# Kernel optimization log

Measured on AMD Instinct MI355X. Metric: run time of the kernel, lower is better.

The kernel has to match this reference:

```python
import jax, jax.numpy as jnp
import numpy as np

N = 40000; E = 512000; F = 128; H = 4; C = 32; HC = 128; G = 64; FC = 48


def _bn(x, g, b):
    # BatchNorm1d in training mode: batch stats, biased variance, eps=1e-5
    mu = jnp.mean(x, 0)
    var = jnp.var(x, 0)
    return g * (x - mu) * jax.lax.rsqrt(var + 1e-5) + b


def _gat(x, src, dst, W, a_s, a_d, bias):
    # PyG GATConv: linear -> per-head edge scores -> self-loops -> LeakyReLU ->
    # segment softmax over incoming edges of each target -> weighted scatter-add
    n = x.shape[0]
    h = (x @ W).reshape(n, H, C)
    es = jnp.einsum('nhc,hc->nh', h, a_s)  # source-side score
    ed = jnp.einsum('nhc,hc->nh', h, a_d)  # target-side score
    loop = jnp.arange(n, dtype=src.dtype)
    s = jnp.concatenate([src, loop])
    d = jnp.concatenate([dst, loop])
    e = jax.nn.leaky_relu(es[s] + ed[d], 0.2)  # [E+N, H]
    m = jax.ops.segment_max(e, d, num_segments=n)
    ex = jnp.exp(e - m[d])
    den = jax.ops.segment_sum(ex, d, num_segments=n)
    alpha = ex / den[d]
    out = jax.ops.segment_sum(h[s] * alpha[:, :, None], d, num_segments=n)
    return out.reshape(n, H * C) + bias


def _pool(x, batch, aw, ab):
    # graph_attention_pool: per-graph softmax over node scores, weighted scatter-add
    sc = x @ aw + ab  # [N,1]
    m = jax.ops.segment_max(sc, batch, num_segments=G)
    ex = jnp.exp(sc - m[batch])
    den = jax.ops.segment_sum(ex, batch, num_segments=G)
    a = ex / den[batch]
    return jax.ops.segment_sum(x * a, batch, num_segments=G)  # [G, HC]


def _forward(x1, x2, W0, as0, ad0, b0, W1, as1, ad1, b1, W2, as2, ad2, b2,
             g1, be1, g2, be2, g3, be3, att_w, att_b, fci_w, fci_b, gbi, bbi,
             fcw, fcb, fc1w, fc1b, gf1, bf1, fc2w, fc2b,
             edge_index1, batch1, edge_index2, batch2):
    def branch(x, ei):
        src, dst = ei[0], ei[1]
        x = jax.nn.relu(_bn(_gat(x, src, dst, W0, as0, ad0, b0), g1, be1))
        x = jax.nn.relu(_bn(_gat(x, src, dst, W1, as1, ad1, b1), g2, be2))
        x = jax.nn.relu(_bn(_gat(x, src, dst, W2, as2, ad2, b2), g3, be3))
        return x
    h1 = branch(x1, edge_index1)
    h2 = branch(x2, edge_index2)
    def head(h, batch):
        p = _pool(h, batch, att_w, att_b)
        z = jax.nn.relu(_bn(p @ fci_w + fci_b, gbi, bbi))
        return z @ fcw + fcb  # note: bn_fc is never applied in the source forward
    o = jnp.concatenate([head(h1, batch1), head(h2, batch2)], axis=-1)
    o = jax.nn.relu(_bn(o @ fc1w + fc1b, gf1, bf1))
    o = o @ fc2w + fc2b
    return jax.nn.sigmoid(o).squeeze(-1)  # [G]


def setup_inputs() -> dict:
    key = jax.random.key(0)
    ks = jax.random.split(key, 24)
    def rn(i, shape, scale=1.0):
        return jax.random.normal(ks[i], shape, jnp.float32) * scale
    inp = {}
    inp['x1'] = rn(0, (N, F))
    inp['x2'] = rn(1, (N, F))
    inp['edge_index1'] = jax.random.randint(ks[2], (2, E), 0, N, dtype=jnp.int32)
    inp['edge_index2'] = jax.random.randint(ks[3], (2, E), 0, N, dtype=jnp.int32)
    inp['batch1'] = jnp.sort(jax.random.randint(ks[4], (N,), 0, G, dtype=jnp.int32))
    inp['batch2'] = jnp.sort(jax.random.randint(ks[5], (N,), 0, G, dtype=jnp.int32))
    inp['W0'] = rn(6, (F, HC), F ** -0.5)
    inp['as0'] = rn(7, (H, C), C ** -0.5)
    inp['ad0'] = rn(8, (H, C), C ** -0.5)
    inp['b0'] = jnp.zeros((HC,), jnp.float32)
    inp['W1'] = rn(9, (HC, HC), HC ** -0.5)
    inp['as1'] = rn(10, (H, C), C ** -0.5)
    inp['ad1'] = rn(11, (H, C), C ** -0.5)
    inp['b1'] = jnp.zeros((HC,), jnp.float32)
    inp['W2'] = rn(12, (HC, HC), HC ** -0.5)
    inp['as2'] = rn(13, (H, C), C ** -0.5)
    inp['ad2'] = rn(14, (H, C), C ** -0.5)
    inp['b2'] = jnp.zeros((HC,), jnp.float32)
    for nm, dim in (('g1', HC), ('g2', HC), ('g3', HC), ('gbi', FC), ('gf1', FC // 4)):
        inp[nm] = jnp.ones((dim,), jnp.float32)
    for nm, dim in (('be1', HC), ('be2', HC), ('be3', HC), ('bbi', FC), ('bf1', FC // 4)):
        inp[nm] = jnp.zeros((dim,), jnp.float32)
    inp['att_w'] = rn(15, (HC, 1), HC ** -0.5)
    inp['att_b'] = jnp.zeros((1,), jnp.float32)
    inp['fci_w'] = rn(16, (HC, FC), HC ** -0.5)
    inp['fci_b'] = jnp.zeros((FC,), jnp.float32)
    inp['fcw'] = rn(17, (FC, FC // 4), FC ** -0.5)
    inp['fcb'] = jnp.zeros((FC // 4,), jnp.float32)
    inp['fc1w'] = rn(18, (FC // 4 * 2, FC // 4), (FC // 2) ** -0.5)
    inp['fc1b'] = jnp.zeros((FC // 4,), jnp.float32)
    inp['fc2w'] = rn(19, (FC // 4, 1), (FC // 4) ** -0.5)
    inp['fc2b'] = jnp.zeros((1,), jnp.float32)
    return inp


def reference(x1, x2, edge_index1, edge_index2, batch1, batch2,
              W0, as0, ad0, b0, W1, as1, ad1, b1, W2, as2, ad2, b2,
              g1, g2, g3, gbi, gf1, be1, be2, be3, bbi, bf1,
              att_w, att_b, fci_w, fci_b, fcw, fcb, fc1w, fc1b, fc2w, fc2b):
    return _forward(x1, x2, W0, as0, ad0, b0, W1, as1, ad1, b1, W2, as2, ad2, b2,
                    g1, be1, g2, be2, g3, be3, att_w, att_b, fci_w, fci_b, gbi, bbi,
                    fcw, fcb, fc1w, fc1b, gf1, bf1, fc2w, fc2b,
                    edge_index1, batch1, edge_index2, batch2)
```

## Files before the change

kernel.cpp:

```cpp
#include <hip/hip_runtime.h>

#define NN 40000
#define EE 512000
#define NB 157
#define BCAP 8000

typedef unsigned short u16;
typedef __attribute__((ext_vector_type(8))) short bf16x8;
typedef __attribute__((ext_vector_type(4))) float f32x4;

__device__ __forceinline__ float bf2f(u16 u) { return __uint_as_float(((unsigned)u) << 16); }
__device__ __forceinline__ u16 f2bf(float f) {
    unsigned u = __float_as_uint(f);
    u += 0x7FFFu + ((u >> 16) & 1u);
    return (u16)(u >> 16);
}
__device__ __forceinline__ unsigned pack2(float a, float b) {
    return (unsigned)f2bf(a) | ((unsigned)f2bf(b) << 16);
}
__device__ __forceinline__ float lrelu(float t) { return t > 0.f ? t : 0.2f * t; }

__global__ __launch_bounds__(256) void detect_k(const u16* __restrict__ x, int* __restrict__ flag) {
    int t = threadIdx.x;
    int cnt = 0;
    for (int j = 0; j < 8; ++j) {
        float v = bf2f(x[(t * 8 + j) * 2]);
        float a = fabsf(v);
        if (a >= 0.00390625f && a <= 256.0f) cnt++;
    }
    __shared__ int sh[256];
    sh[t] = cnt;
    __syncthreads();
    for (int off = 128; off > 0; off >>= 1) {
        if (t < off) sh[t] += sh[t + off];
        __syncthreads();
    }
    if (t == 0) flag[0] = (sh[0] > 1024) ? 1 : 0;
}

struct CvtArgs {
    const void* src[28];
    float* dst[28];
    int n[28];
};

__global__ __launch_bounds__(256) void cvt_k(CvtArgs a, const int* __restrict__ flag) {
    int b = blockIdx.x;
    int n = a.n[b];
    float* d = a.dst[b];
    if (*flag) {
        const u16* p = (const u16*)a.src[b];
        for (int i = threadIdx.x; i < n; i += 256) d[i] = bf2f(p[i]);
    } else {
        const float* p = (const float*)a.src[b];
        for (int i = threadIdx.x; i < n; i += 256) d[i] = p[i];
    }
}

__global__ __launch_bounds__(256) void wtb_k(const float* __restrict__ wcvt, u16* __restrict__ Wtb) {
    int l = blockIdx.x;
    const float* W = wcvt + l * 16640;
    u16* D = Wtb + l * 16384;
    for (int i = threadIdx.x; i < 16384; i += 256) {
        int n = i >> 7, k = i & 127;
        D[i] = f2bf(W[k * 128 + n]);
    }
}

__global__ __launch_bounds__(256) void bucket_k(const int* __restrict__ ei,
                                                int* __restrict__ gcnt,
                                                int2* __restrict__ buf) {
    __shared__ int lh[NB];
    __shared__ int lbase[NB];
    __shared__ int loff[NB];
    int tid = threadIdx.x;
    for (int i = tid; i < NB; i += 256) lh[i] = 0;
    __syncthreads();
    int e0 = blockIdx.x * 1024 + tid;
    int sv[4], dv[4], bv[4];
#pragma unroll
    for (int j = 0; j < 4; ++j) {
        int e = e0 + j * 256;
        int d = ei[EE + e];
        int s = ei[e];
        if ((unsigned)d >= NN) d = -1;
        if ((unsigned)s >= NN) s = 0;
        dv[j] = d;
        sv[j] = s;
        bv[j] = d >> 8;
        if (d >= 0 && (unsigned)bv[j] < NB) atomicAdd(&lh[bv[j]], 1);
        else dv[j] = -1;
    }
    __syncthreads();
    for (int i = tid; i < NB; i += 256) {
        int c = lh[i];
        lbase[i] = c ? atomicAdd(&gcnt[i], c) : 0;
        loff[i] = 0;
    }
    __syncthreads();
#pragma unroll
    for (int j = 0; j < 4; ++j) {
        if (dv[j] >= 0) {
            int b = bv[j];
            int p = lbase[b] + atomicAdd(&loff[b], 1);
            if ((unsigned)p < BCAP) buf[b * BCAP + p] = (int2){sv[j], dv[j]};
        }
    }
}

__global__ __launch_bounds__(256) void build_k(const int* __restrict__ gcnt,
                                               const int2* __restrict__ buf,
                                               int* __restrict__ fill,
                                               int* __restrict__ csrc) {
    __shared__ int lf[256];
    int b = blockIdx.x, tid = threadIdx.x;
    lf[tid] = 0;
    __syncthreads();
    int n = gcnt[b];
    if (n < 0) n = 0;
    if (n > BCAP) n = BCAP;
    int d0 = b << 8;
    for (int i = tid; i < n; i += 256) {
        int2 p = buf[b * BCAP + i];
        unsigned loc = (unsigned)(p.y - d0);
        if (loc < 256u && (unsigned)p.y < NN && (unsigned)p.x < NN) {
            int pos = atomicAdd(&lf[loc], 1);
            if ((unsigned)pos < 64u) csrc[(size_t)p.y * 64 + pos] = p.x;
        }
    }
    __syncthreads();
    int d = d0 + tid;
    if (d < NN) fill[d] = lf[tid];
}

__global__ __launch_bounds__(256) void matmul_mfma_k(const void* __restrict__ Xv, int mode,
                                                     const int* __restrict__ flag,
                                                     const float* __restrict__ bkt,
                                                     const float* __restrict__ gam,
                                                     const float* __restrict__ bet,
                                                     const u16* __restrict__ Wtb,
                                                     const float* __restrict__ asf,
                                                     const float* __restrict__ adf,
                                                     u16* __restrict__ Yb,
                                                     float* __restrict__ es, float* __restrict__ ed) {
    __shared__ u16 Xs[64 * 136];
    __shared__ float red[256];
    __shared__ float scs[128], shs[128];
    int tid = threadIdx.x;
    size_t row0 = (size_t)blockIdx.x * 64;
    if (mode == 1) {
        float s = 0.f;
        for (int b = 0; b < 64; ++b) s += bkt[b * 256 + tid];
        red[tid] = s;
        __syncthreads();
        if (tid < 128) {
            float mu = red[tid] * (1.0f / NN);
            float var = red[128 + tid] * (1.0f / NN) - mu * mu;
            float sc_ = rsqrtf(var + 1e-5f) * gam[tid];
            scs[tid] = sc_;
            shs[tid] = bet[tid] - mu * sc_;
        }
        __syncthreads();
        const uint2* X2 = reinterpret_cast<const uint2*>((const u16*)Xv + row0 * 128);
        for (int i = tid; i < 2048; i += 256) {
            uint2 p = X2[i];
            int r = i >> 5, c0 = (i & 31) * 4;
            float v0 = fmaf(bf2f((u16)(p.x & 0xffffu)), scs[c0], shs[c0]);
            float v1 = fmaf(bf2f((u16)(p.x >> 16)), scs[c0 + 1], shs[c0 + 1]);
            float v2 = fmaf(bf2f((u16)(p.y & 0xffffu)), scs[c0 + 2], shs[c0 + 2]);
            float v3 = fmaf(bf2f((u16)(p.y >> 16)), scs[c0 + 3], shs[c0 + 3]);
            v0 = v0 > 0.f ? v0 : 0.f; v1 = v1 > 0.f ? v1 : 0.f;
            v2 = v2 > 0.f ? v2 : 0.f; v3 = v3 > 0.f ? v3 : 0.f;
            unsigned* dst = (unsigned*)(Xs + r * 136 + c0);
            dst[0] = pack2(v0, v1);
            dst[1] = pack2(v2, v3);
        }
    } else if (*flag) {
        const uint2* X2 = reinterpret_cast<const uint2*>((const u16*)Xv + row0 * 128);
        for (int i = tid; i < 2048; i += 256) {
            uint2 p = X2[i];
            int r = i >> 5, c0 = (i & 31) * 4;
            unsigned* dst = (unsigned*)(Xs + r * 136 + c0);
            dst[0] = p.x;
            dst[1] = p.y;
        }
    } else {
        const float4* X4 = reinterpret_cast<const float4*>((const float*)Xv + row0 * 128);
        for (int i = tid; i < 2048; i += 256) {
            float4 v = X4[i];
            int r = i >> 5, c0 = (i & 31) * 4;
            unsigned* dst = (unsigned*)(Xs + r * 136 + c0);
            dst[0] = pack2(v.x, v.y);
            dst[1] = pack2(v.z, v.w);
        }
    }
    __syncthreads();
    int w = tid >> 6, l = tid & 63;
    int q = l >> 4, c = l & 15;
    int mrow = w * 16;
    f32x4 acc[8];
#pragma unroll
    for (int t = 0; t < 8; ++t) acc[t] = (f32x4){0.f, 0.f, 0.f, 0.f};
#pragma unroll
    for (int ks = 0; ks < 4; ++ks) {
        int k0 = ks * 32;
        bf16x8 afrag = *(const bf16x8*)(Xs + (mrow + c) * 136 + k0 + q * 8);
#pragma unroll
        for (int t = 0; t < 8; ++t) {
            bf16x8 bfrag = *(const bf16x8*)(Wtb + (t * 16 + c) * 128 + k0 + q * 8);
            acc[t] = __builtin_amdgcn_mfma_f32_16x16x32_bf16(afrag, bfrag, acc[t], 0, 0, 0);
        }
    }
    float esp[4][4] = {}, edp[4][4] = {};
#pragma unroll
    for (int t = 0; t < 8; ++t) {
        float av = asf[t * 16 + c], dv = adf[t * 16 + c];
        int h = t >> 1;
#pragma unroll
        for (int r = 0; r < 4; ++r) {
            esp[h][r] = fmaf(acc[t][r], av, esp[h][r]);
            edp[h][r] = fmaf(acc[t][r], dv, edp[h][r]);
        }
    }
#pragma unroll
    for (int h = 0; h < 4; ++h)
#pragma unroll
        for (int r = 0; r < 4; ++r) {
            esp[h][r] += __shfl_xor(esp[h][r], 1, 64);
            esp[h][r] += __shfl_xor(esp[h][r], 2, 64);
            esp[h][r] += __shfl_xor(esp[h][r], 4, 64);
            esp[h][r] += __shfl_xor(esp[h][r], 8, 64);
            edp[h][r] += __shfl_xor(edp[h][r], 1, 64);
            edp[h][r] += __shfl_xor(edp[h][r], 2, 64);
            edp[h][r] += __shfl_xor(edp[h][r], 4, 64);
            edp[h][r] += __shfl_xor(edp[h][r], 8, 64);
        }
    if (c < 4) {
#pragma unroll
        for (int r = 0; r < 4; ++r) {
            size_t row = row0 + mrow + q * 4 + r;
            es[row * 4 + c] = esp[c][r];
            ed[row * 4 + c] = edp[c][r];
        }
    }
    __syncthreads();
    u16* Cs = Xs;
#pragma unroll
    for (int t = 0; t < 8; ++t)
#pragma unroll
        for (int r = 0; r < 4; ++r)
            Cs[(mrow + q * 4 + r) * 128 + t * 16 + c] = f2bf(acc[t][r]);
    __syncthreads();
    uint2* yp = (uint2*)(Yb + row0 * 128);
    const uint2* cs2 = (const uint2*)Cs;
    for (int i = tid; i < 2048; i += 256) yp[i] = cs2[i];
}

__global__ __launch_bounds__(256) void agg_k(const u16* __restrict__ hb, const float* __restrict__ es,
                                             const float* __restrict__ ed, const int* __restrict__ fill,
                                             const int* __restrict__ csrc, u16* __restrict__ Ab,
                                             float* __restrict__ bkt) {
    __shared__ float ss[512], qq[512];
    int wid = (blockIdx.x * 256 + threadIdx.x) >> 6;
    int lane = threadIdx.x & 63;
    int deg = fill[wid];
    if (deg > 64) deg = 64;
    if (deg < 0) deg = 0;
    int rs = wid * 64;
    int head = lane >> 4;
    float edn = ed[wid * 4 + head];
    float acc0, acc1, den;
    {
        float w = __expf(lrelu(es[wid * 4 + head] + edn));
        den = w;
        unsigned pv = ((const unsigned*)(hb + (size_t)wid * 128))[lane];
        acc0 = w * bf2f((u16)(pv & 0xffffu));
        acc1 = w * bf2f((u16)(pv >> 16));
    }
    int i = 0;
    for (; i + 8 <= deg; i += 8) {
        int sv[8];
#pragma unroll
        for (int j = 0; j < 8; ++j) sv[j] = csrc[rs + i + j];
        float wv[8];
#pragma unroll
        for (int j = 0; j < 8; ++j) wv[j] = __expf(lrelu(es[sv[j] * 4 + head] + edn));
        unsigned pv[8];
#pragma unroll
        for (int j = 0; j < 8; ++j) pv[j] = ((const unsigned*)(hb + (size_t)sv[j] * 128))[lane];
#pragma unroll
        for (int j = 0; j < 8; ++j) {
            den += wv[j];
            acc0 = fmaf(wv[j], bf2f((u16)(pv[j] & 0xffffu)), acc0);
            acc1 = fmaf(wv[j], bf2f((u16)(pv[j] >> 16)), acc1);
        }
    }
    for (; i < deg; ++i) {
        int s = csrc[rs + i];
        float w = __expf(lrelu(es[s * 4 + head] + edn));
        den += w;
        unsigned pv = ((const unsigned*)(hb + (size_t)s * 128))[lane];
        acc0 = fmaf(w, bf2f((u16)(pv & 0xffffu)), acc0);
        acc1 = fmaf(w, bf2f((u16)(pv >> 16)), acc1);
    }
    float inv = 1.0f / den;
    float v0 = acc0 * inv, v1 = acc1 * inv;
    ((unsigned*)Ab)[(size_t)wid * 64 + lane] = (unsigned)f2bf(v0) | ((unsigned)f2bf(v1) << 16);
    int w = threadIdx.x >> 6;
    ss[w * 128 + 2 * lane] = v0;      ss[w * 128 + 2 * lane + 1] = v1;
    qq[w * 128 + 2 * lane] = v0 * v0; qq[w * 128 + 2 * lane + 1] = v1 * v1;
    __syncthreads();
    int t = threadIdx.x;
    float* dst = bkt + (blockIdx.x & 63) * 256;
    if (t < 128) {
        atomicAdd(&dst[t], ss[t] + ss[128 + t] + ss[256 + t] + ss[384 + t]);
    } else {
        int f = t - 128;
        atomicAdd(&dst[t], qq[f] + qq[128 + f] + qq[256 + f] + qq[384 + f]);
    }
}

__global__ __launch_bounds__(256) void bnconst_k(const float* __restrict__ bkt,
                                                 const float* __restrict__ gam,
                                                 const float* __restrict__ bet,
                                                 float* __restrict__ bnc) {
    __shared__ float red[256];
    int tid = threadIdx.x;
    float s = 0.f;
    for (int b = 0; b < 64; ++b) s += bkt[b * 256 + tid];
    red[tid] = s;
    __syncthreads();
    if (tid < 128) {
        float mu = red[tid] * (1.0f / NN);
        float var = red[128 + tid] * (1.0f / NN) - mu * mu;
        float sc_ = rsqrtf(var + 1e-5f) * gam[tid];
        bnc[tid] = sc_;
        bnc[128 + tid] = bet[tid] - mu * sc_;
    }
}

__global__ __launch_bounds__(256) void pool_score_k(const u16* __restrict__ Ab,
                                                    const float* __restrict__ bnc,
                                                    const float* __restrict__ attw,
                                                    float* __restrict__ scw) {
    int tid = threadIdx.x;
    int wid = (blockIdx.x * 256 + tid) >> 6;
    int lane = tid & 63;
    int f0 = 2 * lane, f1 = 2 * lane + 1;
    unsigned pv = ((const unsigned*)Ab)[(size_t)wid * 64 + lane];
    float v0 = fmaf(bf2f((u16)(pv & 0xffffu)), bnc[f0], bnc[128 + f0]); v0 = v0 > 0.f ? v0 : 0.f;
    float v1 = fmaf(bf2f((u16)(pv >> 16)), bnc[f1], bnc[128 + f1]);     v1 = v1 > 0.f ? v1 : 0.f;
    float v = v0 * attw[f0] + v1 * attw[f1];
    for (int off = 1; off < 64; off <<= 1) v += __shfl_xor(v, off, 64);
    if (lane == 0) scw[wid] = __expf(v);
}

__device__ __forceinline__ int lower_bound_dev(const int* __restrict__ b, int n, int v) {
    int lo = 0, hi = n;
    while (lo < hi) {
        int mid = (lo + hi) >> 1;
        if (b[mid] < v) lo = mid + 1; else hi = mid;
    }
    return lo;
}

__global__ __launch_bounds__(256) void pool_den_k(const float* __restrict__ scw,
                                                  const int* __restrict__ batch,
                                                  float* __restrict__ gden) {
    int g = blockIdx.x;
    int tid = threadIdx.x;
    int start = lower_bound_dev(batch, NN, g);
    int end = lower_bound_dev(batch, NN, g + 1);
    __shared__ float sh[256];
    float s = 0.f;
    for (int i = start + tid; i < end; i += 256) s += scw[i];
    sh[tid] = s;
    __syncthreads();
    for (int off = 128; off > 0; off >>= 1) {
        if (tid < off) sh[tid] += sh[tid + off];
        __syncthreads();
    }
    if (tid == 0) gden[g] = (sh[0] > 1e-30f) ? sh[0] : 1e-30f;
}

__global__ __launch_bounds__(256) void pool_accum2_k(const u16* __restrict__ Ab,
                                                     const float* __restrict__ scw,
                                                     const int* __restrict__ batch,
                                                     const float* __restrict__ gden,
                                                     const float* __restrict__ bnc,
                                                     float* __restrict__ pooled) {
    __shared__ float wsh[64];
    __shared__ int gsh[64];
    int r0 = blockIdx.x * 64;
    int tid = threadIdx.x;
    if (tid < 64) {
        int g = batch[r0 + tid];
        if ((unsigned)g >= 64) g = 0;
        gsh[tid] = g;
        wsh[tid] = scw[r0 + tid] / gden[g];
    }
    __syncthreads();
    int f = tid & 127, half = tid >> 7;
    float bs = bnc[f], bb = bnc[128 + f];
    float racc = 0.f;
    int curg = gsh[half];
    for (int r = half; r < 64; r += 2) {
        int g = gsh[r];
        if (g != curg) {
            atomicAdd(&pooled[curg * 128 + f], racc);
            racc = 0.f;
            curg = g;
        }
        float v = fmaf(bf2f(Ab[(size_t)(r0 + r) * 128 + f]), bs, bb);
        v = v > 0.f ? v : 0.f;
        racc = fmaf(wsh[r], v, racc);
    }
    atomicAdd(&pooled[curg * 128 + f], racc);
}

__global__ __launch_bounds__(256) void headA_k(const float* __restrict__ pooled,
                                               const float* __restrict__ fciw, const float* __restrict__ fcib,
                                               float* __restrict__ Tall) {
    __shared__ float Wl[6144];
    __shared__ float Pl[128];
    int tid = threadIdx.x;
    int g = blockIdx.x;
    for (int i = tid; i < 6144; i += 256) Wl[i] = fciw[i];
    if (tid < 128) Pl[tid] = pooled[g * 128 + tid];
    __syncthreads();
    if (tid < 48) {
        float s = fcib[tid];
        for (int k = 0; k < 128; ++k) s = fmaf(Pl[k], Wl[k * 48 + tid], s);
        Tall[g * 48 + tid] = s;
    }
}

__global__ __launch_bounds__(256) void headB_k(const float* __restrict__ Tall,
                                               const float* __restrict__ gbi, const float* __restrict__ bbi,
                                               const float* __restrict__ fcw, const float* __restrict__ fcb,
                                               const float* __restrict__ fc1w, const float* __restrict__ fc1b,
                                               const float* __restrict__ gf1, const float* __restrict__ bf1,
                                               const float* __restrict__ fc2w, const float* __restrict__ fc2b,
                                               void* __restrict__ out, const int* __restrict__ flag) {
    __shared__ float T[6144];
    __shared__ float X[64 * 24];
    __shared__ float Y[64 * 12];
    __shared__ float st[192];
    __shared__ float st2[24];
    __shared__ float wl[576 + 288 + 12 + 12 + 12 + 12 + 48 + 48 + 1];
    float* fcw_l  = wl;
    float* fc1w_l = wl + 576;
    float* fcb_l  = wl + 864;
    float* fc1b_l = wl + 876;
    float* gf1_l  = wl + 888;
    float* bf1_l  = wl + 900;
    float* gbi_l  = wl + 912;
    float* bbi_l  = wl + 960;
    float* fc2b_l = wl + 1008;
    __shared__ float fc2w_l[12];
    int tid = threadIdx.x;
    for (int i = tid; i < 6144; i += 256) T[i] = Tall[i];
    for (int i = tid; i < 576; i += 256) fcw_l[i] = fcw[i];
    for (int i = tid; i < 288; i += 256) fc1w_l[i] = fc1w[i];
    if (tid < 12) {
        fcb_l[tid] = fcb[tid]; fc1b_l[tid] = fc1b[tid];
        gf1_l[tid] = gf1[tid]; bf1_l[tid] = bf1[tid];
        fc2w_l[tid] = fc2w[tid];
    }
    if (tid < 48) { gbi_l[tid] = gbi[tid]; bbi_l[tid] = bbi[tid]; }
    if (tid == 0) fc2b_l[0] = fc2b[0];
    __syncthreads();
    if (tid < 96) {
        int b = tid / 48, c = tid - b * 48;
        float s = 0.f, ss = 0.f;
        for (int g = 0; g < 64; ++g) { float v = T[b * 3072 + g * 48 + c]; s += v; ss += v * v; }
        float mu = s * (1.f / 64), var = ss * (1.f / 64) - mu * mu;
        float sc_ = rsqrtf(var + 1e-5f) * gbi_l[c];
        st[tid] = sc_;
        st[96 + tid] = bbi_l[c] - mu * sc_;
    }
    __syncthreads();
    for (int i = tid; i < 6144; i += 256) {
        int b = i / 3072, c = i % 48;
        int col = b * 48 + c;
        float v = fmaf(T[i], st[col], st[96 + col]);
        T[i] = v > 0.f ? v : 0.f;
    }
    __syncthreads();
    for (int idx = tid; idx < 1536; idx += 256) {
        int b = idx / 768, r = idx - b * 768;
        int g = r / 12, c = r - g * 12;
        float s = fcb_l[c];
        const float* tr = T + b * 3072 + g * 48;
        for (int k = 0; k < 48; ++k) s = fmaf(tr[k], fcw_l[k * 12 + c], s);
        X[g * 24 + b * 12 + c] = s;
    }
    __syncthreads();
    for (int idx = tid; idx < 768; idx += 256) {
        int g = idx / 12, c = idx - g * 12;
        float s = fc1b_l[c];
        const float* xr = X + g * 24;
        for (int k = 0; k < 24; ++k) s = fmaf(xr[k], fc1w_l[k * 12 + c], s);
        Y[idx] = s;
    }
    __syncthreads();
    if (tid < 12) {
        float s = 0.f, ss = 0.f;
        for (int g = 0; g < 64; ++g) { float v = Y[g * 12 + tid]; s += v; ss += v * v; }
        float mu = s * (1.f / 64), var = ss * (1.f / 64) - mu * mu;
        float sc_ = rsqrtf(var + 1e-5f) * gf1_l[tid];
        st2[tid] = sc_;
        st2[12 + tid] = bf1_l[tid] - mu * sc_;
    }
    __syncthreads();
    if (tid < 64) {
        float s = fc2b_l[0];
        for (int k = 0; k < 12; ++k) {
            float v = fmaf(Y[tid * 12 + k], st2[k], st2[12 + k]);
            v = v > 0.f ? v : 0.f;
            s = fmaf(v, fc2w_l[k], s);
        }
        float sig = 1.f / (1.f + __expf(-s));
        if (*flag) ((u16*)out)[tid] = f2bf(sig);
        else       ((float*)out)[tid] = sig;
    }
}

extern "C" void kernel_launch(void* const* d_in, const int* in_sizes, int n_in,
                              void* d_out, int out_size, void* d_ws, size_t ws_size,
                              hipStream_t stream) {
    const void* xin[2]  = {d_in[0], d_in[1]};
    const int* ei[2]    = {(const int*)d_in[2], (const int*)d_in[3]};
    const int* batch[2] = {(const int*)d_in[4], (const int*)d_in[5]};

    char* ws = (char*)d_ws;
    u16*   Hb     = (u16*)(ws + 0);
    u16*   Ab     = (u16*)(ws + 10240000);
    float* es     = (float*)(ws + 20480000);
    float* ed     = (float*)(ws + 21120000);
    float* scw    = (float*)(ws + 21760000);
    int*   fill   = (int*)(ws + 21920000);
    int*   csrc   = (int*)(ws + 22080000);
    float* wcvt   = (float*)(ws + 32320000);
    u16*   Wtb    = (u16*)(ws + 32560000);
    float* zbase  = (float*)(ws + 32658304);
    float* bkt    = zbase;
    float* pooled = zbase + 98304;
    float* gden   = pooled + 16384;
    float* bnc    = gden + 128;
    float* Tall   = bnc + 256;
    int*   flag   = (int*)(Tall + 6144);
    int*   gcnt   = (int*)scw;

    static const int widx[28] = {6,7,8, 10,11,12, 14,15,16, 18,19,20, 23,24,25,
                                 21,26, 22,27, 28, 30,31, 32,33, 34,35, 36,37};
    static const int wn[28]   = {16384,128,128, 16384,128,128, 16384,128,128, 128,128,128,
                                 128,128,128, 48,48, 12,12, 128, 6144,48, 576,12, 288,12, 12,1};
    CvtArgs ca;
    float* wptr[28];
    {
        size_t off = 0;
        for (int i = 0; i < 28; ++i) {
            ca.src[i] = d_in[widx[i]];
            ca.dst[i] = wcvt + off;
            ca.n[i] = wn[i];
            wptr[i] = wcvt + off;
            off += wn[i];
        }
    }
    const float* asf[3] = {wptr[1], wptr[4], wptr[7]};
    const float* adf[3] = {wptr[2], wptr[5], wptr[8]};
    const float* gf[3]  = {wptr[9], wptr[10], wptr[11]};
    const float* bef[3] = {wptr[12], wptr[13], wptr[14]};
    const float *gbi = wptr[15], *bbi = wptr[16], *gf1 = wptr[17], *bf1 = wptr[18];
    const float *attw = wptr[19], *fciw = wptr[20], *fcib = wptr[21];
    const float *fcw = wptr[22], *fcb = wptr[23], *fc1w = wptr[24], *fc1b = wptr[25];
    const float *fc2w = wptr[26], *fc2b = wptr[27];

    detect_k<<<1, 256, 0, stream>>>((const u16*)d_in[0], flag);
    cvt_k<<<28, 256, 0, stream>>>(ca, flag);
    wtb_k<<<3, 256, 0, stream>>>(wcvt, Wtb);
    (void)hipMemsetAsync(zbase, 0, (98304 + 16384) * sizeof(float), stream);

    for (int b = 0; b < 2; ++b) {
        (void)hipMemsetAsync(gcnt, 0, NB * sizeof(int), stream);
        bucket_k<<<500, 256, 0, stream>>>(ei[b], gcnt, (int2*)Hb);
        build_k<<<NB, 256, 0, stream>>>(gcnt, (const int2*)Hb, fill, csrc);
        for (int l = 0; l < 3; ++l) {
            float* bktl = bkt + (b * 3 + l) * 16384;
            float* bktprev = bkt + (b * 3 + l - 1) * 16384;
            matmul_mfma_k<<<625, 256, 0, stream>>>(l == 0 ? xin[b] : (const void*)Ab,
                                                   l == 0 ? 0 : 1, flag,
                                                   l == 0 ? bkt : bktprev,
                                                   l == 0 ? gf[0] : gf[l - 1],
                                                   l == 0 ? bef[0] : bef[l - 1],
                                                   Wtb + l * 16384, asf[l], adf[l], Hb, es, ed);
            agg_k<<<10000, 256, 0, stream>>>(Hb, es, ed, fill, csrc, Ab, bktl);
        }
        float* bkt3 = bkt + (b * 3 + 2) * 16384;
        bnconst_k<<<1, 256, 0, stream>>>(bkt3, gf[2], bef[2], bnc);
        pool_score_k<<<10000, 256, 0, stream>>>(Ab, bnc, attw, scw);
        pool_den_k<<<64, 256, 0, stream>>>(scw, batch[b], gden + b * 64);
        pool_accum2_k<<<625, 256, 0, stream>>>(Ab, scw, batch[b], gden + b * 64,
                                               bnc, pooled + b * 8192);
        headA_k<<<64, 256, 0, stream>>>(pooled + b * 8192, fciw, fcib, Tall + b * 3072);
    }
    headB_k<<<1, 256, 0, stream>>>(Tall, gbi, bbi, fcw, fcb, fc1w, fc1b, gf1, bf1,
                                   fc2w, fc2b, d_out, flag);
}
```

Before: 689.2 us.

## Batch both graph branches into single kernel launches per stage

Processes the two independent graph branches together: every stage (bucketing, CSR build, matmul, aggregation, pooling, head) launches once with twice the blocks, and each block picks its branch from its block index. Workspace buffers are doubled to hold both branches at once. BN constants are now computed by a separate small kernel after each layer instead of being recomputed inside every matmul block. This removes half the launches and gives small kernels more parallel work, at the cost of a larger workspace footprint.

```diff
diff --git a/kernel.cpp b/kernel.cpp
--- a/kernel.cpp
+++ b/kernel.cpp
@@ -67,16 +67,21 @@
     }
 }
 
-__global__ __launch_bounds__(256) void bucket_k(const int* __restrict__ ei,
+__global__ __launch_bounds__(256) void bucket_k(const int* __restrict__ ei1,
+                                                const int* __restrict__ ei2,
                                                 int* __restrict__ gcnt,
                                                 int2* __restrict__ buf) {
     __shared__ int lh[NB];
     __shared__ int lbase[NB];
     __shared__ int loff[NB];
+    int branch = blockIdx.x >= 500;
+    int blk = blockIdx.x - (branch ? 500 : 0);
+    const int* ei = branch ? ei2 : ei1;
+    int gb0 = branch * NB;
     int tid = threadIdx.x;
     for (int i = tid; i < NB; i += 256) lh[i] = 0;
     __syncthreads();
-    int e0 = blockIdx.x * 1024 + tid;
+    int e0 = blk * 1024 + tid;
     int sv[4], dv[4], bv[4];
 #pragma unroll
     for (int j = 0; j < 4; ++j) {
@@ -94,7 +99,7 @@
     __syncthreads();
     for (int i = tid; i < NB; i += 256) {
         int c = lh[i];
-        lbase[i] = c ? atomicAdd(&gcnt[i], c) : 0;
+        lbase[i] = c ? atomicAdd(&gcnt[gb0 + i], c) : 0;
         loff[i] = 0;
     }
     __syncthreads();
@@ -103,7 +108,7 @@
         if (dv[j] >= 0) {
             int b = bv[j];
             int p = lbase[b] + atomicAdd(&loff[b], 1);
-            if ((unsigned)p < BCAP) buf[b * BCAP + p] = (int2){sv[j], dv[j]};
+            if ((unsigned)p < BCAP) buf[(size_t)(gb0 + b) * BCAP + p] = (int2){sv[j], dv[j]};
         }
     }
 }
@@ -113,57 +118,57 @@
                                                int* __restrict__ fill,
                                                int* __restrict__ csrc) {
     __shared__ int lf[256];
-    int b = blockIdx.x, tid = threadIdx.x;
+    int branch = blockIdx.x >= NB;
+    int b = blockIdx.x - (branch ? NB : 0);
+    int tid = threadIdx.x;
     lf[tid] = 0;
     __syncthreads();
-    int n = gcnt[b];
+    int n = gcnt[branch * NB + b];
     if (n < 0) n = 0;
     if (n > BCAP) n = BCAP;
     int d0 = b << 8;
+    size_t soff = (size_t)branch * NN;
+    const int2* bp = buf + (size_t)(branch * NB + b) * BCAP;
     for (int i = tid; i < n; i += 256) {
-        int2 p = buf[b * BCAP + i];
+        int2 p = bp[i];
         unsigned loc = (unsigned)(p.y - d0);
         if (loc < 256u && (unsigned)p.y < NN && (unsigned)p.x < NN) {
             int pos = atomicAdd(&lf[loc], 1);
-            if ((unsigned)pos < 64u) csrc[(size_t)p.y * 64 + pos] = p.x;
+            if ((unsigned)pos < 64u) csrc[(soff + p.y) * 64 + pos] = p.x;
         }
     }
     __syncthreads();
     int d = d0 + tid;
-    if (d < NN) fill[d] = lf[tid];
-}
-
-__global__ __launch_bounds__(256) void matmul_mfma_k(const void* __restrict__ Xv, int mode,
+    if (d < NN) fill[soff + d] = lf[tid];
+}
+
+__global__ __launch_bounds__(256) void matmul_mfma_k(const void* __restrict__ X1,
+                                                     const void* __restrict__ X2,
+                                                     const u16* __restrict__ Abase,
+                                                     int mode,
                                                      const int* __restrict__ flag,
-                                                     const float* __restrict__ bkt,
-                                                     const float* __restrict__ gam,
-                                                     const float* __restrict__ bet,
+                                                     const float* __restrict__ bnc,
                                                      const u16* __restrict__ Wtb,
                                                      const float* __restrict__ asf,
                                                      const float* __restrict__ adf,
-                                                     u16* __restrict__ Yb,
+                                                     u16* __restrict__ Hbase,
                                                      float* __restrict__ es, float* __restrict__ ed) {
     __shared__ u16 Xs[64 * 136];
-    __shared__ float red[256];
     __shared__ float scs[128], shs[128];
     int tid = threadIdx.x;
-    size_t row0 = (size_t)blockIdx.x * 64;
+    int branch = blockIdx.x >= 625;
+    int blk = blockIdx.x - (branch ? 625 : 0);
+    size_t boff = (size_t)branch * NN;
+    size_t row0 = (size_t)blk * 64;
     if (mode == 1) {
-        float s = 0.f;
-        for (int b = 0; b < 64; ++b) s += bkt[b * 256 + tid];
-        red[tid] = s;
+        if (tid < 128) {
+            scs[tid] = bnc[branch * 256 + tid];
+            shs[tid] = bnc[branch * 256 + 128 + tid];
+        }
         __syncthreads();
-        if (tid < 128) {
-            float mu = red[tid] * (1.0f / NN);
-            float var = red[128 + tid] * (1.0f / NN) - mu * mu;
-            float sc_ = rsqrtf(var + 1e-5f) * gam[tid];
-            scs[tid] = sc_;
-            shs[tid] = bet[tid] - mu * sc_;
-        }
-        __syncthreads();
-        const uint2* X2 = reinterpret_cast<const uint2*>((const u16*)Xv + row0 * 128);
+        const uint2* X2p = reinterpret_cast<const uint2*>(Abase + (boff + row0) * 128);
         for (int i = tid; i < 2048; i += 256) {
-            uint2 p = X2[i];
+            uint2 p = X2p[i];
             int r = i >> 5, c0 = (i & 31) * 4;
             float v0 = fmaf(bf2f((u16)(p.x & 0xffffu)), scs[c0], shs[c0]);
             float v1 = fmaf(bf2f((u16)(p.x >> 16)), scs[c0 + 1], shs[c0 + 1]);
@@ -175,23 +180,26 @@
             dst[0] = pack2(v0, v1);
             dst[1] = pack2(v2, v3);
         }
-    } else if (*flag) {
-        const uint2* X2 = reinterpret_cast<const uint2*>((const u16*)Xv + row0 * 128);
-        for (int i = tid; i < 2048; i += 256) {
-            uint2 p = X2[i];
-            int r = i >> 5, c0 = (i & 31) * 4;
-            unsigned* dst = (unsigned*)(Xs + r * 136 + c0);
-            dst[0] = p.x;
-            dst[1] = p.y;
-        }
     } else {
-        const float4* X4 = reinterpret_cast<const float4*>((const float*)Xv + row0 * 128);
-        for (int i = tid; i < 2048; i += 256) {
-            float4 v = X4[i];
-            int r = i >> 5, c0 = (i & 31) * 4;
-            unsigned* dst = (unsigned*)(Xs + r * 136 + c0);
-            dst[0] = pack2(v.x, v.y);
-            dst[1] = pack2(v.z, v.w);
+        const void* Xv = branch ? X2 : X1;
+        if (*flag) {
+            const uint2* X2p = reinterpret_cast<const uint2*>((const u16*)Xv + row0 * 128);
+            for (int i = tid; i < 2048; i += 256) {
+                uint2 p = X2p[i];
+                int r = i >> 5, c0 = (i & 31) * 4;
+                unsigned* dst = (unsigned*)(Xs + r * 136 + c0);
+                dst[0] = p.x;
+                dst[1] = p.y;
+            }
+        } else {
+            const float4* X4 = reinterpret_cast<const float4*>((const float*)Xv + row0 * 128);
+            for (int i = tid; i < 2048; i += 256) {
+                float4 v = X4[i];
+                int r = i >> 5, c0 = (i & 31) * 4;
+                unsigned* dst = (unsigned*)(Xs + r * 136 + c0);
+                dst[0] = pack2(v.x, v.y);
+                dst[1] = pack2(v.z, v.w);
+            }
         }
     }
     __syncthreads();
@@ -238,9 +246,9 @@
     if (c < 4) {
 #pragma unroll
         for (int r = 0; r < 4; ++r) {
-            size_t row = row0 + mrow + q * 4 + r;
-            es[row * 4 + c] = esp[c][r];
-            ed[row * 4 + c] = edp[c][r];
+            size_t grow = boff + row0 + mrow + q * 4 + r;
+            es[grow * 4 + c] = esp[c][r];
+            ed[grow * 4 + c] = edp[c][r];
         }
     }
     __syncthreads();
@@ -251,7 +259,7 @@
         for (int r = 0; r < 4; ++r)
             Cs[(mrow + q * 4 + r) * 128 + t * 16 + c] = f2bf(acc[t][r]);
     __syncthreads();
-    uint2* yp = (uint2*)(Yb + row0 * 128);
+    uint2* yp = (uint2*)(Hbase + (boff + row0) * 128);
     const uint2* cs2 = (const uint2*)Cs;
     for (int i = tid; i < 2048; i += 256) yp[i] = cs2[i];
 }
@@ -259,21 +267,23 @@
 __global__ __launch_bounds__(256) void agg_k(const u16* __restrict__ hb, const float* __restrict__ es,
                                              const float* __restrict__ ed, const int* __restrict__ fill,
                                              const int* __restrict__ csrc, u16* __restrict__ Ab,
-                                             float* __restrict__ bkt) {
+                                             float* __restrict__ bktbase, int l) {
     __shared__ float ss[512], qq[512];
-    int wid = (blockIdx.x * 256 + threadIdx.x) >> 6;
+    int gwid = (blockIdx.x * 256 + threadIdx.x) >> 6;
+    int branch = gwid >= NN;
+    size_t srow = branch ? (size_t)NN : 0;
     int lane = threadIdx.x & 63;
-    int deg = fill[wid];
+    int deg = fill[gwid];
     if (deg > 64) deg = 64;
     if (deg < 0) deg = 0;
-    int rs = wid * 64;
+    size_t rs = (size_t)gwid * 64;
     int head = lane >> 4;
-    float edn = ed[wid * 4 + head];
+    float edn = ed[gwid * 4 + head];
     float acc0, acc1, den;
     {
-        float w = __expf(lrelu(es[wid * 4 + head] + edn));
+        float w = __expf(lrelu(es[gwid * 4 + head] + edn));
         den = w;
-        unsigned pv = ((const unsigned*)(hb + (size_t)wid * 128))[lane];
+        unsigned pv = ((const unsigned*)(hb + (size_t)gwid * 128))[lane];
         acc0 = w * bf2f((u16)(pv & 0xffffu));
         acc1 = w * bf2f((u16)(pv >> 16));
     }
@@ -284,10 +294,10 @@
         for (int j = 0; j < 8; ++j) sv[j] = csrc[rs + i + j];
         float wv[8];
 #pragma unroll
-        for (int j = 0; j < 8; ++j) wv[j] = __expf(lrelu(es[sv[j] * 4 + head] + edn));
+        for (int j = 0; j < 8; ++j) wv[j] = __expf(lrelu(es[(srow + sv[j]) * 4 + head] + edn));
         unsigned pv[8];
 #pragma unroll
-        for (int j = 0; j < 8; ++j) pv[j] = ((const unsigned*)(hb + (size_t)sv[j] * 128))[lane];
+        for (int j = 0; j < 8; ++j) pv[j] = ((const unsigned*)(hb + (srow + sv[j]) * 128))[lane];
 #pragma unroll
         for (int j = 0; j < 8; ++j) {
             den += wv[j];
@@ -297,21 +307,21 @@
     }
     for (; i < deg; ++i) {
         int s = csrc[rs + i];
-        float w = __expf(lrelu(es[s * 4 + head] + edn));
+        float w = __expf(lrelu(es[(srow + s) * 4 + head] + edn));
         den += w;
-        unsigned pv = ((const unsigned*)(hb + (size_t)s * 128))[lane];
+        unsigned pv = ((const unsigned*)(hb + (srow + s) * 128))[lane];
         acc0 = fmaf(w, bf2f((u16)(pv & 0xffffu)), acc0);
         acc1 = fmaf(w, bf2f((u16)(pv >> 16)), acc1);
     }
     float inv = 1.0f / den;
     float v0 = acc0 * inv, v1 = acc1 * inv;
-    ((unsigned*)Ab)[(size_t)wid * 64 + lane] = (unsigned)f2bf(v0) | ((unsigned)f2bf(v1) << 16);
+    ((unsigned*)Ab)[(size_t)gwid * 64 + lane] = (unsigned)f2bf(v0) | ((unsigned)f2bf(v1) << 16);
     int w = threadIdx.x >> 6;
     ss[w * 128 + 2 * lane] = v0;      ss[w * 128 + 2 * lane + 1] = v1;
     qq[w * 128 + 2 * lane] = v0 * v0; qq[w * 128 + 2 * lane + 1] = v1 * v1;
     __syncthreads();
     int t = threadIdx.x;
-    float* dst = bkt + (blockIdx.x & 63) * 256;
+    float* dst = bktbase + (branch * 3 + l) * 16384 + (blockIdx.x & 63) * 256;
     if (t < 128) {
         atomicAdd(&dst[t], ss[t] + ss[128 + t] + ss[256 + t] + ss[384 + t]);
     } else {
@@ -320,22 +330,24 @@
     }
 }
 
-__global__ __launch_bounds__(256) void bnconst_k(const float* __restrict__ bkt,
+__global__ __launch_bounds__(256) void bnconst_k(const float* __restrict__ bktbase, int l,
                                                  const float* __restrict__ gam,
                                                  const float* __restrict__ bet,
                                                  float* __restrict__ bnc) {
     __shared__ float red[256];
+    int b = blockIdx.x;
+    const float* bkt = bktbase + (b * 3 + l) * 16384;
     int tid = threadIdx.x;
     float s = 0.f;
-    for (int b = 0; b < 64; ++b) s += bkt[b * 256 + tid];
+    for (int k = 0; k < 64; ++k) s += bkt[k * 256 + tid];
     red[tid] = s;
     __syncthreads();
     if (tid < 128) {
         float mu = red[tid] * (1.0f / NN);
         float var = red[128 + tid] * (1.0f / NN) - mu * mu;
         float sc_ = rsqrtf(var + 1e-5f) * gam[tid];
-        bnc[tid] = sc_;
-        bnc[128 + tid] = bet[tid] - mu * sc_;
+        bnc[b * 256 + tid] = sc_;
+        bnc[b * 256 + 128 + tid] = bet[tid] - mu * sc_;
     }
 }
 
@@ -344,15 +356,17 @@
                                                     const float* __restrict__ attw,
                                                     float* __restrict__ scw) {
     int tid = threadIdx.x;
-    int wid = (blockIdx.x * 256 + tid) >> 6;
+    int gwid = (blockIdx.x * 256 + tid) >> 6;
+    int branch = gwid >= NN;
+    const float* bncp = bnc + branch * 256;
     int lane = tid & 63;
     int f0 = 2 * lane, f1 = 2 * lane + 1;
-    unsigned pv = ((const unsigned*)Ab)[(size_t)wid * 64 + lane];
-    float v0 = fmaf(bf2f((u16)(pv & 0xffffu)), bnc[f0], bnc[128 + f0]); v0 = v0 > 0.f ? v0 : 0.f;
-    float v1 = fmaf(bf2f((u16)(pv >> 16)), bnc[f1], bnc[128 + f1]);     v1 = v1 > 0.f ? v1 : 0.f;
+    unsigned pv = ((const unsigned*)Ab)[(size_t)gwid * 64 + lane];
+    float v0 = fmaf(bf2f((u16)(pv & 0xffffu)), bncp[f0], bncp[128 + f0]); v0 = v0 > 0.f ? v0 : 0.f;
+    float v1 = fmaf(bf2f((u16)(pv >> 16)), bncp[f1], bncp[128 + f1]);     v1 = v1 > 0.f ? v1 : 0.f;
     float v = v0 * attw[f0] + v1 * attw[f1];
     for (int off = 1; off < 64; off <<= 1) v += __shfl_xor(v, off, 64);
-    if (lane == 0) scw[wid] = __expf(v);
+    if (lane == 0) scw[gwid] = __expf(v);
 }
 
 __device__ __forceinline__ int lower_bound_dev(const int* __restrict__ b, int n, int v) {
@@ -365,57 +379,68 @@
 }
 
 __global__ __launch_bounds__(256) void pool_den_k(const float* __restrict__ scw,
-                                                  const int* __restrict__ batch,
+                                                  const int* __restrict__ batch1,
+                                                  const int* __restrict__ batch2,
                                                   float* __restrict__ gden) {
-    int g = blockIdx.x;
+    int branch = blockIdx.x >= 64;
+    int g = blockIdx.x - (branch ? 64 : 0);
+    const int* batch = branch ? batch2 : batch1;
+    const float* sc = scw + (size_t)branch * NN;
     int tid = threadIdx.x;
     int start = lower_bound_dev(batch, NN, g);
     int end = lower_bound_dev(batch, NN, g + 1);
     __shared__ float sh[256];
     float s = 0.f;
-    for (int i = start + tid; i < end; i += 256) s += scw[i];
+    for (int i = start + tid; i < end; i += 256) s += sc[i];
     sh[tid] = s;
     __syncthreads();
     for (int off = 128; off > 0; off >>= 1) {
         if (tid < off) sh[tid] += sh[tid + off];
         __syncthreads();
     }
-    if (tid == 0) gden[g] = (sh[0] > 1e-30f) ? sh[0] : 1e-30f;
+    if (tid == 0) gden[blockIdx.x] = (sh[0] > 1e-30f) ? sh[0] : 1e-30f;
 }
 
 __global__ __launch_bounds__(256) void pool_accum2_k(const u16* __restrict__ Ab,
                                                      const float* __restrict__ scw,
-                                                     const int* __restrict__ batch,
+                                                     const int* __restrict__ batch1,
+                                                     const int* __restrict__ batch2,
                                                      const float* __restrict__ gden,
                                                      const float* __restrict__ bnc,
                                                      float* __restrict__ pooled) {
     __shared__ float wsh[64];
     __shared__ int gsh[64];
-    int r0 = blockIdx.x * 64;
+    int branch = blockIdx.x >= 625;
+    int blk = blockIdx.x - (branch ? 625 : 0);
+    const int* batch = branch ? batch2 : batch1;
+    size_t boff = (size_t)branch * NN;
+    int r0 = blk * 64;
     int tid = threadIdx.x;
     if (tid < 64) {
         int g = batch[r0 + tid];
         if ((unsigned)g >= 64) g = 0;
         gsh[tid] = g;
-        wsh[tid] = scw[r0 + tid] / gden[g];
-    }
-    __syncthreads();
+        wsh[tid] = scw[boff + r0 + tid] / gden[branch * 64 + g];
+    }
+    __syncthreads();
+    const float* bncp = bnc + branch * 256;
+    float* poolp = pooled + (size_t)branch * 8192;
     int f = tid & 127, half = tid >> 7;
-    float bs = bnc[f], bb = bnc[128 + f];
+    float bs = bncp[f], bb = bncp[128 + f];
     float racc = 0.f;
     int curg = gsh[half];
     for (int r = half; r < 64; r += 2) {
         int g = gsh[r];
         if (g != curg) {
-            atomicAdd(&pooled[curg * 128 + f], racc);
+            atomicAdd(&poolp[curg * 128 + f], racc);
             racc = 0.f;
             curg = g;
         }
-        float v = fmaf(bf2f(Ab[(size_t)(r0 + r) * 128 + f]), bs, bb);
+        float v = fmaf(bf2f(Ab[(boff + r0 + r) * 128 + f]), bs, bb);
         v = v > 0.f ? v : 0.f;
         racc = fmaf(wsh[r], v, racc);
     }
-    atomicAdd(&pooled[curg * 128 + f], racc);
+    atomicAdd(&poolp[curg * 128 + f], racc);
 }
 
 __global__ __launch_bounds__(256) void headA_k(const float* __restrict__ pooled,
@@ -535,22 +560,22 @@
 
     char* ws = (char*)d_ws;
     u16*   Hb     = (u16*)(ws + 0);
-    u16*   Ab     = (u16*)(ws + 10240000);
-    float* es     = (float*)(ws + 20480000);
-    float* ed     = (float*)(ws + 21120000);
-    float* scw    = (float*)(ws + 21760000);
-    int*   fill   = (int*)(ws + 21920000);
-    int*   csrc   = (int*)(ws + 22080000);
-    float* wcvt   = (float*)(ws + 32320000);
-    u16*   Wtb    = (u16*)(ws + 32560000);
-    float* zbase  = (float*)(ws + 32658304);
+    u16*   Ab     = (u16*)(ws + 20480000);
+    float* es     = (float*)(ws + 40960000);
+    float* ed     = (float*)(ws + 42240000);
+    float* scw    = (float*)(ws + 43520000);
+    int*   fill   = (int*)(ws + 43840000);
+    int*   csrc   = (int*)(ws + 44160000);
+    float* wcvt   = (float*)(ws + 64640000);
+    u16*   Wtb    = (u16*)(ws + 64880000);
+    float* zbase  = (float*)(ws + 64978304);
     float* bkt    = zbase;
     float* pooled = zbase + 98304;
-    float* gden   = pooled + 16384;
-    float* bnc    = gden + 128;
-    float* Tall   = bnc + 256;
-    int*   flag   = (int*)(Tall + 6144);
-    int*   gcnt   = (int*)scw;
+    int*   gcnt   = (int*)(zbase + 114688);
+    float* gden   = zbase + 115008;
+    float* bnc    = zbase + 115136;
+    float* Tall   = zbase + 115648;
+    int*   flag   = (int*)(zbase + 121792);
 
     static const int widx[28] = {6,7,8, 10,11,12, 14,15,16, 18,19,20, 23,24,25,
                                  21,26, 22,27, 28, 30,31, 32,33, 34,35, 36,37};
@@ -580,31 +605,22 @@
     detect_k<<<1, 256, 0, stream>>>((const u16*)d_in[0], flag);
     cvt_k<<<28, 256, 0, stream>>>(ca, flag);
     wtb_k<<<3, 256, 0, stream>>>(wcvt, Wtb);
-    (void)hipMemsetAsync(zbase, 0, (98304 + 16384) * sizeof(float), stream);
-
-    for (int b = 0; b < 2; ++b) {
-        (void)hipMemsetAsync(gcnt, 0, NB * sizeof(int), stream);
-        bucket_k<<<500, 256, 0, stream>>>(ei[b], gcnt, (int2*)Hb);
-        build_k<<<NB, 256, 0, stream>>>(gcnt, (const int2*)Hb, fill, csrc);
-        for (int l = 0; l < 3; ++l) {
-            float* bktl = bkt + (b * 3 + l) * 16384;
-            float* bktprev = bkt + (b * 3 + l - 1) * 16384;
-            matmul_mfma_k<<<625, 256, 0, stream>>>(l == 0 ? xin[b] : (const void*)Ab,
-                                                   l == 0 ? 0 : 1, flag,
-                                                   l == 0 ? bkt : bktprev,
-                                                   l == 0 ? gf[0] : gf[l - 1],
-                                                   l == 0 ? bef[0] : bef[l - 1],
-                                                   Wtb + l * 16384, asf[l], adf[l], Hb, es, ed);
-            agg_k<<<10000, 256, 0, stream>>>(Hb, es, ed, fill, csrc, Ab, bktl);
-        }
-        float* bkt3 = bkt + (b * 3 + 2) * 16384;
-        bnconst_k<<<1, 256, 0, stream>>>(bkt3, gf[2], bef[2], bnc);
-        pool_score_k<<<10000, 256, 0, stream>>>(Ab, bnc, attw, scw);
-        pool_den_k<<<64, 256, 0, stream>>>(scw, batch[b], gden + b * 64);
-        pool_accum2_k<<<625, 256, 0, stream>>>(Ab, scw, batch[b], gden + b * 64,
-                                               bnc, pooled + b * 8192);
-        headA_k<<<64, 256, 0, stream>>>(pooled + b * 8192, fciw, fcib, Tall + b * 3072);
-    }
+    (void)hipMemsetAsync(zbase, 0, (98304 + 16384 + 320) * sizeof(float), stream);
+
+    bucket_k<<<1000, 256, 0, stream>>>(ei[0], ei[1], gcnt, (int2*)Hb);
+    build_k<<<2 * NB, 256, 0, stream>>>(gcnt, (const int2*)Hb, fill, csrc);
+
+    for (int l = 0; l < 3; ++l) {
+        matmul_mfma_k<<<1250, 256, 0, stream>>>(xin[0], xin[1], Ab, l == 0 ? 0 : 1, flag,
+                                                bnc, Wtb + l * 16384, asf[l], adf[l],
+                                                Hb, es, ed);
+        agg_k<<<20000, 256, 0, stream>>>(Hb, es, ed, fill, csrc, Ab, bkt, l);
+        bnconst_k<<<2, 256, 0, stream>>>(bkt, l, gf[l], bef[l], bnc);
+    }
+    pool_score_k<<<20000, 256, 0, stream>>>(Ab, bnc, attw, scw);
+    pool_den_k<<<128, 256, 0, stream>>>(scw, batch[0], batch[1], gden);
+    pool_accum2_k<<<1250, 256, 0, stream>>>(Ab, scw, batch[0], batch[1], gden, bnc, pooled);
+    headA_k<<<128, 256, 0, stream>>>(pooled, fciw, fcib, Tall);
     headB_k<<<1, 256, 0, stream>>>(Tall, gbi, bbi, fcw, fcb, fc1w, fc1b, gf1, bf1,
                                    fc2w, fc2b, d_out, flag);
 }
```

New measurement: 589.5 us (median of 2 runs). 1.17x faster.
